# Kernel tuning notes

Measured on AMD Instinct MI355X. Metric: run time of the kernel, lower is better.

Reference implementation:

```python
import jax, jax.numpy as jnp
import numpy as np
from jax import lax

C = 512          # in_channels
L = 4            # fcos_conv_layers
NUM_CLS = 1      # fcos_num_class - 1
PRIOR_BIAS = float(-np.log((1 - 0.01) / 0.01))
BN_EPS = 1e-5


def conv1d(x, w, b, pad):
    # x: [B, Cin, T], w: [Cout, Cin, K]
    y = lax.conv_general_dilated(x, w, window_strides=(1,), padding=[(pad, pad)],
                                 dimension_numbers=('NCH', 'OIH', 'NCH'))
    return y + b[None, :, None]


def bn(x, g, b, m, v):
    inv = lax.rsqrt(v + BN_EPS)
    return (x - m[None, :, None]) * (g * inv)[None, :, None] + b[None, :, None]


def tower(x, ws, bs, gs, bes, ms, vs):
    # ws: [L, C, C, 3]; fixed small loop over layers
    for i in range(L):
        x = jax.nn.relu(bn(conv1d(x, ws[i], bs[i], 1), gs[i], bes[i], ms[i], vs[i]))
    return x


def setup_inputs() -> dict:
    key = jax.random.key(0)
    ks = jax.random.split(key, 32)
    d = {}
    d['f0'] = jax.random.normal(ks[0], (8, C, 1024), jnp.float32)
    d['f1'] = jax.random.normal(ks[1], (8, C, 512), jnp.float32)
    d['f2'] = jax.random.normal(ks[2], (8, C, 256), jnp.float32)

    def nrm(k, shape):
        return 0.01 * jax.random.normal(k, shape, jnp.float32)

    # cls / bbox towers: stacked conv + BN params
    d['cls_tw_w'] = nrm(ks[3], (L, C, C, 3)); d['cls_tw_b'] = jnp.zeros((L, C))
    d['cls_bn_g'] = jnp.ones((L, C)); d['cls_bn_b'] = jnp.zeros((L, C))
    d['cls_bn_m'] = jnp.zeros((L, C)); d['cls_bn_v'] = jnp.ones((L, C))
    d['box_tw_w'] = nrm(ks[4], (L, C, C, 3)); d['box_tw_b'] = jnp.zeros((L, C))
    d['box_bn_g'] = jnp.ones((L, C)); d['box_bn_b'] = jnp.zeros((L, C))
    d['box_bn_m'] = jnp.zeros((L, C)); d['box_bn_v'] = jnp.ones((L, C))

    d['logits_w'] = nrm(ks[5], (NUM_CLS, C, 3))
    d['logits_b'] = jnp.full((NUM_CLS,), PRIOR_BIAS, jnp.float32)
    d['bbox_w'] = nrm(ks[6], (2, C, 3)); d['bbox_b'] = jnp.zeros((2,))

    d['mix_w'] = nrm(ks[7], (C, 2 * C, 1)); d['mix_b'] = jnp.zeros((C,))
    d['mix_bn_g'] = jnp.ones((C,)); d['mix_bn_b'] = jnp.zeros((C,))
    d['mix_bn_m'] = jnp.zeros((C,)); d['mix_bn_v'] = jnp.ones((C,))

    d['iou_w1'] = nrm(ks[8], (C // 2, C, 3)); d['iou_b1'] = jnp.zeros((C // 2,))
    d['iou_bn_g'] = jnp.ones((C // 2,)); d['iou_bn_b'] = jnp.zeros((C // 2,))
    d['iou_bn_m'] = jnp.zeros((C // 2,)); d['iou_bn_v'] = jnp.ones((C // 2,))
    d['iou_w2'] = nrm(ks[9], (1, C // 2, 1)); d['iou_b2'] = jnp.zeros((1,))

    d['scales'] = jnp.ones((3,), jnp.float32)
    return d


def reference(f0, f1, f2,
              cls_tw_w, cls_tw_b, cls_bn_g, cls_bn_b, cls_bn_m, cls_bn_v,
              box_tw_w, box_tw_b, box_bn_g, box_bn_b, box_bn_m, box_bn_v,
              logits_w, logits_b, bbox_w, bbox_b,
              mix_w, mix_b, mix_bn_g, mix_bn_b, mix_bn_m, mix_bn_v,
              iou_w1, iou_b1, iou_bn_g, iou_bn_b, iou_bn_m, iou_bn_v,
              iou_w2, iou_b2, scales):
    outs = []
    for l, x in enumerate([f0, f1, f2]):
        ct = tower(x, cls_tw_w, cls_tw_b, cls_bn_g, cls_bn_b, cls_bn_m, cls_bn_v)
        bt = tower(x, box_tw_w, box_tw_b, box_bn_g, box_bn_b, box_bn_m, box_bn_v)
        logits = conv1d(ct, logits_w, logits_b, 1)                      # [B, 1, T]
        bbox = jnp.exp(conv1d(bt, bbox_w, bbox_b, 1) * scales[l])       # [B, 2, T]
        mix = jax.nn.relu(bn(conv1d(jnp.concatenate([ct, bt], axis=1), mix_w, mix_b, 0),
                             mix_bn_g, mix_bn_b, mix_bn_m, mix_bn_v))   # [B, C, T]
        h = jax.nn.relu(bn(conv1d(mix, iou_w1, iou_b1, 1),
                           iou_bn_g, iou_bn_b, iou_bn_m, iou_bn_v))
        iou = conv1d(h, iou_w2, iou_b2, 0)                              # [B, 1, T]
        outs.append(jnp.concatenate([logits, bbox, iou], axis=1))       # [B, 4, T]
    return jnp.concatenate(outs, axis=-1)  # [B, 4, T0+T1+T2]
```

## Files before the change

kernel.cpp:

```cpp
#include <hip/hip_runtime.h>
#include <hip/hip_bf16.h>


typedef __bf16 bf16x8 __attribute__((ext_vector_type(8)));
typedef float f32x4 __attribute__((ext_vector_type(4)));

__device__ __forceinline__ float bf2f(unsigned short u) {
    union { unsigned int i; float f; } c; c.i = ((unsigned int)u) << 16; return c.f;
}
__device__ __forceinline__ unsigned short f2bf(float f) {
    union { __hip_bfloat16 h; unsigned short u; } c; c.h = __float2bfloat16(f); return c.u;
}

__device__ __forceinline__ void gload16(const void* g, void* l) {
    __builtin_amdgcn_global_load_lds(
        (const __attribute__((address_space(1))) unsigned int*)g,
        (__attribute__((address_space(3))) unsigned int*)l,
        16, 0, 0);
}

__device__ __forceinline__ void tile_decode(int ct, int& rowstart, int& t0, int& Tl) {
    if (ct < 64)      { Tl = 1024; int b = ct >> 3;                 t0 = (ct & 7) << 7; rowstart = b * 1026 + 1; }
    else if (ct < 96) { Tl = 512;  int i = ct - 64; int b = i >> 2; t0 = (i & 3) << 7; rowstart = 8208 + b * 514 + 1; }
    else              { Tl = 256;  int i = ct - 96; int b = i >> 1; t0 = (i & 1) << 7; rowstart = 12320 + b * 258 + 1; }
}

template<int KSIZE>
__global__ __launch_bounds__(256)
void conv_gemm(const unsigned short* __restrict__ X, int xstride, int ci0_base, int ci_twstride, int Cin,
               const unsigned short* __restrict__ W, int w_twstride,
               const float* __restrict__ Bs, int b_twstride,
               unsigned short* __restrict__ Y, int ystride, int co_twstride,
               int relu)
{
    constexpr int BM = 128, BN = 128, BK = 32;
    constexpr int NR = BN + KSIZE - 1;
    constexpr int XSEG = (NR * 64 + 1023) / 1024;
    constexpr int XPW  = (XSEG + 3) / 4;
    constexpr int WSEG = KSIZE * BM * 64 / 1024;
    constexpr int WPW  = WSEG / 4;
    __shared__ alignas(16) unsigned short Xs[2 * XSEG * 512];
    __shared__ alignas(16) unsigned short Ws[2 * WSEG * 512];

    const int tid = threadIdx.x;
    const int lane = tid & 63, wid = tid >> 6;
    int rowstart, t0, Tl;
    tile_decode(blockIdx.x, rowstart, t0, Tl);
    const int co0 = blockIdx.y * BM;
    const int tw = blockIdx.z;
    const int ci_off = ci0_base + tw * ci_twstride;
    const unsigned short* Wp = W + (size_t)tw * w_twstride;
    const float* Bp = Bs + tw * b_twstride;
    const int co_out0 = tw * co_twstride + co0;

    const int wm = (wid >> 1) * 64, wn = (wid & 1) * 64;
    const int lr = lane & 15;
    const int sr = lane >> 4;

    const unsigned short* xga[XPW]; unsigned short* xl[XPW];
#pragma unroll
    for (int p = 0; p < XPW; ++p) {
        int seg = (KSIZE == 3) ? ((p < 2) ? p * 4 + wid : 8) : (p * 4 + wid);
        xl[p] = Xs + seg * 512;
        int g = seg * 64 + lane;
        int row = g >> 2, s = (g & 3) ^ ((row >> 1) & 3);
        xga[p] = X + (size_t)(rowstart - (KSIZE >> 1) + row) * xstride + ci_off + s * 8;
    }
    const unsigned short* wga[WPW]; unsigned short* wl[WPW];
#pragma unroll
    for (int p = 0; p < WPW; ++p) {
        int seg = p * 4 + wid;
        wl[p] = Ws + seg * 512;
        int g = seg * 64 + lane;
        int row = g >> 2, s = (g & 3) ^ ((row >> 1) & 3);
        int co = row & (BM - 1), kk = row >> 7;
        wga[p] = Wp + (size_t)(co0 + co) * (KSIZE * Cin) + kk * Cin + s * 8;
    }

    f32x4 acc[4][4];
#pragma unroll
    for (int i = 0; i < 4; ++i)
#pragma unroll
        for (int j = 0; j < 4; ++j) acc[i][j] = (f32x4){0.f, 0.f, 0.f, 0.f};

    auto STAGE = [&](int buf) {
#pragma unroll
        for (int p = 0; p < XPW; ++p) { gload16(xga[p], xl[p] + buf * (XSEG * 512)); xga[p] += BK; }
#pragma unroll
        for (int p = 0; p < WPW; ++p) { gload16(wga[p], wl[p] + buf * (WSEG * 512)); wga[p] += BK; }
    };

    const int nk = Cin / BK;
    STAGE(0);
    int cur = 0;
    for (int ks = 0; ks < nk; ++ks) {
        if (ks + 1 < nk) {
            STAGE(cur ^ 1);
            if constexpr (KSIZE == 3) asm volatile("s_waitcnt vmcnt(9)" ::: "memory");
            else                      asm volatile("s_waitcnt vmcnt(4)" ::: "memory");
        } else {
            asm volatile("s_waitcnt vmcnt(0)" ::: "memory");
        }
        __builtin_amdgcn_sched_barrier(0);
        __builtin_amdgcn_s_barrier();

        const char* bXs = (const char*)Xs + cur * (XSEG * 1024);
        const char* bWs = (const char*)Ws + cur * (WSEG * 1024);
#pragma unroll
        for (int kk = 0; kk < KSIZE; ++kk) {
            bf16x8 af[4], bv[4];
#pragma unroll
            for (int mi = 0; mi < 4; ++mi) {
                int ra = kk * BM + wm + mi * 16 + lr;
                af[mi] = *(const bf16x8*)(bWs + ra * 64 + (((sr ^ (ra >> 1)) & 3) << 4));
                int rb = wn + mi * 16 + lr + kk;
                bv[mi] = *(const bf16x8*)(bXs + rb * 64 + (((sr ^ (rb >> 1)) & 3) << 4));
            }
#pragma unroll
            for (int mi = 0; mi < 4; ++mi)
#pragma unroll
                for (int ni = 0; ni < 4; ++ni)
                    acc[mi][ni] = __builtin_amdgcn_mfma_f32_16x16x32_bf16(af[mi], bv[ni], acc[mi][ni], 0, 0, 0);
        }
        __builtin_amdgcn_sched_barrier(0);
        __builtin_amdgcn_s_barrier();
        cur ^= 1;
    }

    const int r4 = (lane >> 4) * 4;
#pragma unroll
    for (int mi = 0; mi < 4; ++mi) {
        int co_l = wm + mi * 16 + r4;
        float b0 = Bp[co0 + co_l + 0], b1 = Bp[co0 + co_l + 1];
        float b2 = Bp[co0 + co_l + 2], b3 = Bp[co0 + co_l + 3];
#pragma unroll
        for (int ni = 0; ni < 4; ++ni) {
            int t = t0 + wn + ni * 16 + lr;
            f32x4 a = acc[mi][ni];
            float v0 = a[0] + b0, v1 = a[1] + b1, v2 = a[2] + b2, v3 = a[3] + b3;
            if (relu) {
                v0 = fmaxf(v0, 0.f); v1 = fmaxf(v1, 0.f);
                v2 = fmaxf(v2, 0.f); v3 = fmaxf(v3, 0.f);
            }
            union { unsigned long long u; unsigned short s[4]; } pk;
            pk.s[0] = f2bf(v0); pk.s[1] = f2bf(v1); pk.s[2] = f2bf(v2); pk.s[3] = f2bf(v3);
            *(unsigned long long*)(Y + (size_t)(rowstart + t) * ystride + co_out0 + co_l) = pk.u;
        }
    }
}

__global__ __launch_bounds__(256)
void zero_pads(unsigned short* __restrict__ act0, unsigned short* __restrict__ catA,
               unsigned short* __restrict__ catB, unsigned short* __restrict__ mixo,
               unsigned short* __restrict__ iouh)
{
    int c = blockIdx.x >> 1, side = blockIdx.x & 1;
    int start, Tl;
    if (c < 8)       { start = c * 1026;               Tl = 1024; }
    else if (c < 16) { start = 8208 + (c - 8) * 514;   Tl = 512;  }
    else             { start = 12320 + (c - 16) * 258; Tl = 256;  }
    size_t prow = start + (side ? Tl + 1 : 0);
    int tid = threadIdx.x;
    uint4 z = make_uint4(0u, 0u, 0u, 0u);
    if (tid < 64)  *(uint4*)(act0 + prow * 512 + tid * 8) = z;
    if (tid < 128) { *(uint4*)(catA + prow * 1024 + tid * 8) = z;
                     *(uint4*)(catB + prow * 1024 + tid * 8) = z; }
    if (tid >= 128 && tid < 192) *(uint4*)(mixo + prow * 512 + (tid - 128) * 8) = z;
    if (tid >= 192 && tid < 224) *(uint4*)(iouh + prow * 256 + (tid - 192) * 8) = z;
}

__global__ __launch_bounds__(256)
void transpose_in(const float* __restrict__ f0, const float* __restrict__ f1, const float* __restrict__ f2,
                  unsigned short* __restrict__ act0)
{
    __shared__ float tile[32][33];
    int bx = blockIdx.x;
    const float* src; int Tl, padbase, b, t0;
    if (bx < 256)      { src = f0; Tl = 1024; int i = bx;       b = i >> 5; t0 = (i & 31) << 5; padbase = b * 1026; }
    else if (bx < 384) { src = f1; Tl = 512;  int i = bx - 256; b = i >> 4; t0 = (i & 15) << 5; padbase = 8208 + b * 514; }
    else               { src = f2; Tl = 256;  int i = bx - 384; b = i >> 3; t0 = (i & 7)  << 5; padbase = 12320 + b * 258; }
    int c0 = blockIdx.y << 5;
    const float* sb = src + (size_t)b * 512 * Tl;
    int tl = threadIdx.x & 31, cl = threadIdx.x >> 5;
#pragma unroll
    for (int j = 0; j < 4; ++j) {
        int c = cl + j * 8;
        tile[c][tl] = sb[(size_t)(c0 + c) * Tl + t0 + tl];
    }
    __syncthreads();
    int cc = threadIdx.x & 31, tr0 = threadIdx.x >> 5;
    size_t base = (size_t)(padbase + 1 + t0) * 512 + c0;
#pragma unroll
    for (int j = 0; j < 4; ++j) {
        int tr = tr0 + j * 8;
        act0[base + (size_t)tr * 512 + cc] = f2bf(tile[cc][tr]);
    }
}

__global__ __launch_bounds__(256)
void prep_tower(const float* __restrict__ cls_w, const float* __restrict__ box_w,
                const float* __restrict__ cg, const float* __restrict__ cvv,
                const float* __restrict__ bg, const float* __restrict__ bvv,
                unsigned short* __restrict__ Wt)
{
    int idx = blockIdx.x * 256 + threadIdx.x;
    if (idx >= 2 * 4 * 512 * 3 * 512) return;
    int ci = idx & 511;
    int kk = (idx >> 9) % 3;
    int co = (idx / 1536) & 511;
    int l  = (idx / 786432) & 3;
    int tw = idx / 3145728;
    const float* w = tw ? box_w : cls_w;
    const float* g = tw ? bg : cg;
    const float* v = tw ? bvv : cvv;
    float s = g[l * 512 + co] * rsqrtf(v[l * 512 + co] + 1e-5f);
    float val = w[(((size_t)(l * 512 + co)) * 512 + ci) * 3 + kk] * s;
    Wt[idx] = f2bf(val);
}

__global__ __launch_bounds__(256)
void prep_misc(const float* mix_w, const float* mix_b, const float* mg, const float* mbeta, const float* mm, const float* mv,
               const float* iou_w1, const float* iou_b1, const float* ig, const float* ibeta, const float* im, const float* iv,
               const float* cls_b, const float* cg, const float* cbeta, const float* cm, const float* cv2,
               const float* box_b, const float* bg, const float* bbeta, const float* bm, const float* bv2,
               unsigned short* Wmix, unsigned short* Wiou, float* Bt, float* Bmix, float* Biou)
{
    int idx = blockIdx.x * 256 + threadIdx.x;
    if (idx < 524288) {
        int co = idx >> 10;
        float s = mg[co] * rsqrtf(mv[co] + 1e-5f);
        Wmix[idx] = f2bf(mix_w[idx] * s);
        return;
    }
    idx -= 524288;
    if (idx < 393216) {
        int ci = idx & 511, kk = (idx >> 9) % 3, co = idx / 1536;
        float s = ig[co] * rsqrtf(iv[co] + 1e-5f);
        Wiou[idx] = f2bf(iou_w1[((size_t)(co * 512 + ci)) * 3 + kk] * s);
        return;
    }
    idx -= 393216;
    if (idx < 4096) {
        int co = idx & 511, l = (idx >> 9) & 3, tw = idx >> 11;
        const float* g = tw ? bg : cg; const float* v = tw ? bv2 : cv2;
        const float* m = tw ? bm : cm; const float* be = tw ? bbeta : cbeta;
        const float* cb = tw ? box_b : cls_b;
        int o = l * 512 + co;
        float s = g[o] * rsqrtf(v[o] + 1e-5f);
        Bt[idx] = (cb[o] - m[o]) * s + be[o];
        return;
    }
    idx -= 4096;
    if (idx < 512) {
        float s = mg[idx] * rsqrtf(mv[idx] + 1e-5f);
        Bmix[idx] = (mix_b[idx] - mm[idx]) * s + mbeta[idx];
        return;
    }
    idx -= 512;
    if (idx < 256) {
        float s = ig[idx] * rsqrtf(iv[idx] + 1e-5f);
        Biou[idx] = (iou_b1[idx] - im[idx]) * s + ibeta[idx];
    }
}

__global__ __launch_bounds__(256)
void heads_kernel(const unsigned short* __restrict__ catb, const unsigned short* __restrict__ iouh,
                  const float* __restrict__ lw, const float* __restrict__ lb,
                  const float* __restrict__ bw, const float* __restrict__ bb,
                  const float* __restrict__ iw, const float* __restrict__ ib,
                  const float* __restrict__ scales, float* __restrict__ out)
{
    const int lane = threadIdx.x & 63;
    const int wid = threadIdx.x >> 6;

    float lwr[24], bwr0[24], bwr1[24], iwr[4];
    {
        const float4* p = (const float4*)(lw + lane * 24);
#pragma unroll
        for (int q = 0; q < 6; ++q) {
            float4 v = p[q];
            lwr[q * 4 + 0] = v.x; lwr[q * 4 + 1] = v.y; lwr[q * 4 + 2] = v.z; lwr[q * 4 + 3] = v.w;
        }
        p = (const float4*)(bw + lane * 24);
#pragma unroll
        for (int q = 0; q < 6; ++q) {
            float4 v = p[q];
            bwr0[q * 4 + 0] = v.x; bwr0[q * 4 + 1] = v.y; bwr0[q * 4 + 2] = v.z; bwr0[q * 4 + 3] = v.w;
        }
        p = (const float4*)(bw + 1536 + lane * 24);
#pragma unroll
        for (int q = 0; q < 6; ++q) {
            float4 v = p[q];
            bwr1[q * 4 + 0] = v.x; bwr1[q * 4 + 1] = v.y; bwr1[q * 4 + 2] = v.z; bwr1[q * 4 + 3] = v.w;
        }
        float4 v = *(const float4*)(iw + lane * 4);
        iwr[0] = v.x; iwr[1] = v.y; iwr[2] = v.z; iwr[3] = v.w;
    }
    const float lb0 = lb[0], bb0 = bb[0], bb1 = bb[1], ib0 = ib[0];
    const float s0 = scales[0], s1 = scales[1], s2 = scales[2];

    for (int r = blockIdx.x * 4 + wid; r < 14336; r += gridDim.x * 4) {
        int tlog, roff, tgoff, padbase; float sc;
        if (r < 8192)       { tlog = 10; roff = 0;     tgoff = 0;    sc = s0; }
        else if (r < 12288) { tlog = 9;  roff = 8192;  tgoff = 1024; sc = s1; }
        else                { tlog = 8;  roff = 12288; tgoff = 1536; sc = s2; }
        int i = r - roff;
        int Tl = 1 << tlog;
        int b = i >> tlog, t = i & (Tl - 1);
        if (r < 8192)       padbase = b * 1026;
        else if (r < 12288) padbase = 8208 + b * 514;
        else                padbase = 12320 + b * 258;
        int prow = padbase + 1 + t;

        float al = 0.f, a0 = 0.f, a1 = 0.f, ai = 0.f;
        const unsigned short* base = catb + (size_t)prow * 1024 + lane * 8;
#pragma unroll
        for (int kk = 0; kk < 3; ++kk) {
            union { uint4 u; unsigned short s[8]; } cv, bv;
            cv.u = *(const uint4*)(base + (kk - 1) * 1024);
            bv.u = *(const uint4*)(base + (kk - 1) * 1024 + 512);
#pragma unroll
            for (int j = 0; j < 8; ++j) {
                float xc = bf2f(cv.s[j]);
                float xb = bf2f(bv.s[j]);
                al = fmaf(xc, lwr[j * 3 + kk], al);
                a0 = fmaf(xb, bwr0[j * 3 + kk], a0);
                a1 = fmaf(xb, bwr1[j * 3 + kk], a1);
            }
        }
        {
            union { uint2 u; unsigned short s[4]; } hv;
            hv.u = *(const uint2*)(iouh + (size_t)prow * 256 + lane * 4);
#pragma unroll
            for (int j = 0; j < 4; ++j) ai = fmaf(bf2f(hv.s[j]), iwr[j], ai);
        }
#pragma unroll
        for (int off = 32; off > 0; off >>= 1) {
            al += __shfl_xor(al, off);
            a0 += __shfl_xor(a0, off);
            a1 += __shfl_xor(a1, off);
            ai += __shfl_xor(ai, off);
        }
        if (lane == 0) {
            int tg = tgoff + t;
            out[((size_t)b * 4 + 0) * 1792 + tg] = al + lb0;
            out[((size_t)b * 4 + 1) * 1792 + tg] = expf((a0 + bb0) * sc);
            out[((size_t)b * 4 + 2) * 1792 + tg] = expf((a1 + bb1) * sc);
            out[((size_t)b * 4 + 3) * 1792 + tg] = ai + ib0;
        }
    }
}

extern "C" void kernel_launch(void* const* d_in, const int* in_sizes, int n_in,
                              void* d_out, int out_size, void* d_ws, size_t ws_size,
                              hipStream_t stream)
{
    const float* f0       = (const float*)d_in[0];
    const float* f1       = (const float*)d_in[1];
    const float* f2       = (const float*)d_in[2];
    const float* cls_tw_w = (const float*)d_in[3];
    const float* cls_tw_b = (const float*)d_in[4];
    const float* cls_bn_g = (const float*)d_in[5];
    const float* cls_bn_b = (const float*)d_in[6];
    const float* cls_bn_m = (const float*)d_in[7];
    const float* cls_bn_v = (const float*)d_in[8];
    const float* box_tw_w = (const float*)d_in[9];
    const float* box_tw_b = (const float*)d_in[10];
    const float* box_bn_g = (const float*)d_in[11];
    const float* box_bn_b = (const float*)d_in[12];
    const float* box_bn_m = (const float*)d_in[13];
    const float* box_bn_v = (const float*)d_in[14];
    const float* logits_w = (const float*)d_in[15];
    const float* logits_b = (const float*)d_in[16];
    const float* bbox_w   = (const float*)d_in[17];
    const float* bbox_b   = (const float*)d_in[18];
    const float* mix_w    = (const float*)d_in[19];
    const float* mix_b    = (const float*)d_in[20];
    const float* mix_bn_g = (const float*)d_in[21];
    const float* mix_bn_b = (const float*)d_in[22];
    const float* mix_bn_m = (const float*)d_in[23];
    const float* mix_bn_v = (const float*)d_in[24];
    const float* iou_w1   = (const float*)d_in[25];
    const float* iou_b1   = (const float*)d_in[26];
    const float* iou_bn_g = (const float*)d_in[27];
    const float* iou_bn_b = (const float*)d_in[28];
    const float* iou_bn_m = (const float*)d_in[29];
    const float* iou_bn_v = (const float*)d_in[30];
    const float* iou_w2   = (const float*)d_in[31];
    const float* iou_b2   = (const float*)d_in[32];
    const float* scales   = (const float*)d_in[33];

    unsigned char* ws = (unsigned char*)d_ws;
    unsigned short* Wt   = (unsigned short*)(ws + 0);
    unsigned short* Wmix = (unsigned short*)(ws + 12582912);
    unsigned short* Wiou = (unsigned short*)(ws + 13631488);
    float*          Bt   = (float*)(ws + 14417920);
    float*          Bmix = (float*)(ws + 14434304);
    float*          Biou = (float*)(ws + 14436352);
    unsigned short* act0 = (unsigned short*)(ws + 14437376);
    unsigned short* catA = (unsigned short*)(ws + 29182976);
    unsigned short* catB = (unsigned short*)(ws + 58674176);
    unsigned short* mixo = (unsigned short*)(ws + 88165376);
    unsigned short* iouh = (unsigned short*)(ws + 102910976);

    zero_pads<<<dim3(48), dim3(256), 0, stream>>>(act0, catA, catB, mixo, iouh);
    prep_tower<<<dim3(24576), dim3(256), 0, stream>>>(cls_tw_w, box_tw_w, cls_bn_g, cls_bn_v,
                                                      box_bn_g, box_bn_v, Wt);
    prep_misc<<<dim3(3603), dim3(256), 0, stream>>>(mix_w, mix_b, mix_bn_g, mix_bn_b, mix_bn_m, mix_bn_v,
                                                    iou_w1, iou_b1, iou_bn_g, iou_bn_b, iou_bn_m, iou_bn_v,
                                                    cls_tw_b, cls_bn_g, cls_bn_b, cls_bn_m, cls_bn_v,
                                                    box_tw_b, box_bn_g, box_bn_b, box_bn_m, box_bn_v,
                                                    Wmix, Wiou, Bt, Bmix, Biou);
    transpose_in<<<dim3(448, 16), dim3(256), 0, stream>>>(f0, f1, f2, act0);

    conv_gemm<3><<<dim3(112, 4, 2), 256, 0, stream>>>(act0, 512, 0, 0, 512,
                                                      Wt, 3145728, Bt, 2048, catA, 1024, 512, 1);
    conv_gemm<3><<<dim3(112, 4, 2), 256, 0, stream>>>(catA, 1024, 0, 512, 512,
                                                      Wt + 786432, 3145728, Bt + 512, 2048, catB, 1024, 512, 1);
    conv_gemm<3><<<dim3(112, 4, 2), 256, 0, stream>>>(catB, 1024, 0, 512, 512,
                                                      Wt + 1572864, 3145728, Bt + 1024, 2048, catA, 1024, 512, 1);
    conv_gemm<3><<<dim3(112, 4, 2), 256, 0, stream>>>(catA, 1024, 0, 512, 512,
                                                      Wt + 2359296, 3145728, Bt + 1536, 2048, catB, 1024, 512, 1);
    conv_gemm<1><<<dim3(112, 4, 1), 256, 0, stream>>>(catB, 1024, 0, 0, 1024,
                                                      Wmix, 0, Bmix, 0, mixo, 512, 0, 1);
    conv_gemm<3><<<dim3(112, 2, 1), 256, 0, stream>>>(mixo, 512, 0, 0, 512,
                                                      Wiou, 0, Biou, 0, iouh, 256, 0, 1);
    heads_kernel<<<dim3(896), dim3(256), 0, stream>>>(catB, iouh, logits_w, logits_b,
                                                      bbox_w, bbox_b, iou_w2, iou_b2, scales,
                                                      (float*)d_out);
}
```

Measured before the change: 317.2 us.

## Add dedicated 256x256-tile double-buffered conv kernel for tower layers

Replaces the generic 128x128 conv_gemm launches for the four tower layers with a specialized conv_tower kernel. It uses 512 threads, 256 output channels by 256 time steps per block, and double-buffered LDS with swizzled layouts. Weight loads are interleaved across the three kernel taps, and MFMA runs under raised priority. The larger tiles cut redundant global loads and raise MFMA density, and the remapped block index (L&7)*28+(L>>3) spreads work across XCDs. In exchange, each block uses about 130KB of LDS and many registers, which limits occupancy, and the grid shrinks to 224 blocks, which may leave some CUs underused.

```diff
diff --git a/kernel.cpp b/kernel.cpp
--- a/kernel.cpp
+++ b/kernel.cpp
@@ -17,6 +17,137 @@
         (const __attribute__((address_space(1))) unsigned int*)g,
         (__attribute__((address_space(3))) unsigned int*)l,
         16, 0, 0);
+}
+
+__global__ __launch_bounds__(512, 2)
+void conv_tower(const unsigned short* __restrict__ X, int xstride, int ci_twstride,
+                const unsigned short* __restrict__ W,
+                const float* __restrict__ Bs,
+                unsigned short* __restrict__ Y)
+{
+    constexpr int XHALF = 17 * 512;
+    constexpr int WHALF = 48 * 512;
+    __shared__ alignas(16) unsigned short Xs[2 * XHALF];
+    __shared__ alignas(16) unsigned short Wsh[2 * WHALF];
+
+    const int L = blockIdx.x;
+    const int P = (L & 7) * 28 + (L >> 3);
+    const int tt = P >> 2, sub = P & 3;
+    const int tw = sub >> 1, co0 = (sub & 1) << 8;
+
+    int rowstart;
+    if (tt < 32)      { rowstart = (tt >> 2) * 1026 + 1 + ((tt & 3) << 8); }
+    else if (tt < 48) { int i = tt - 32; rowstart = 8208 + (i >> 1) * 514 + 1 + ((i & 1) << 8); }
+    else              { rowstart = 12320 + (tt - 48) * 258 + 1; }
+
+    const int tid = threadIdx.x;
+    const int lane = tid & 63, wid = tid >> 6;
+    const int wco = (wid >> 2) << 7;
+    const int wt  = (wid & 3) << 6;
+    const int lr = lane & 15;
+    const int sr = lane >> 4;
+
+    const unsigned short* Wp = W + (size_t)tw * 3145728;
+    const float* Bp = Bs + tw * 2048;
+    const int co_out0 = tw * 512 + co0;
+    const int ci_off = tw * ci_twstride;
+
+    const unsigned short* xga[3]; unsigned short* xl0[3];
+#pragma unroll
+    for (int p = 0; p < 3; ++p) {
+        int seg = (p < 2) ? (p * 8 + wid) : 16;
+        xl0[p] = Xs + seg * 512;
+        int g = seg * 64 + lane;
+        int row = g >> 2, sc = (g & 3) ^ ((row >> 1) & 3);
+        xga[p] = X + (size_t)(rowstart - 1 + row) * xstride + ci_off + sc * 8;
+    }
+    const unsigned short* wga[6]; unsigned short* wl0[6];
+#pragma unroll
+    for (int p = 0; p < 6; ++p) {
+        int seg = p * 8 + wid;
+        wl0[p] = Wsh + seg * 512;
+        int g = seg * 64 + lane;
+        int row = g >> 2, sc = (g & 3) ^ ((row >> 1) & 3);
+        int co = row & 255, kk = row >> 8;
+        wga[p] = Wp + (size_t)(co0 + co) * 1536 + kk * 512 + sc * 8;
+    }
+
+    f32x4 acc[8][4];
+#pragma unroll
+    for (int i = 0; i < 8; ++i)
+#pragma unroll
+        for (int j = 0; j < 4; ++j) acc[i][j] = (f32x4){0.f, 0.f, 0.f, 0.f};
+
+#pragma unroll
+    for (int p = 0; p < 3; ++p) { gload16(xga[p], xl0[p]); xga[p] += 32; }
+#pragma unroll
+    for (int p = 0; p < 6; ++p) { gload16(wga[p], wl0[p]); wga[p] += 32; }
+    asm volatile("s_waitcnt vmcnt(0)" ::: "memory");
+    __builtin_amdgcn_s_barrier();
+
+    int cur = 0;
+    for (int ks = 0; ks < 16; ++ks) {
+        const bool notlast = (ks < 15);
+        const char* bX = (const char*)Xs + cur * (XHALF * 2);
+        const char* bW = (const char*)Wsh + cur * (WHALF * 2);
+#pragma unroll
+        for (int kk = 0; kk < 3; ++kk) {
+            bf16x8 af[8], bv[4];
+#pragma unroll
+            for (int mi = 0; mi < 8; ++mi) {
+                int ra = kk * 256 + wco + mi * 16 + lr;
+                af[mi] = *(const bf16x8*)(bW + ra * 64 + (((sr ^ (ra >> 1)) & 3) << 4));
+            }
+#pragma unroll
+            for (int ni = 0; ni < 4; ++ni) {
+                int rb = wt + ni * 16 + lr + kk;
+                bv[ni] = *(const bf16x8*)(bX + rb * 64 + (((sr ^ (rb >> 1)) & 3) << 4));
+            }
+            if (notlast) {
+                if (kk == 0) {
+#pragma unroll
+                    for (int p = 0; p < 3; ++p) { gload16(xga[p], xl0[p] + (cur ^ 1) * XHALF); xga[p] += 32; }
+                } else {
+#pragma unroll
+                    for (int p = 0; p < 3; ++p) {
+                        int q = (kk - 1) * 3 + p;
+                        gload16(wga[q], wl0[q] + (cur ^ 1) * WHALF); wga[q] += 32;
+                    }
+                }
+            }
+            __builtin_amdgcn_s_barrier();
+            asm volatile("s_waitcnt lgkmcnt(0)" ::: "memory");
+            __builtin_amdgcn_sched_barrier(0);
+            __builtin_amdgcn_s_setprio(1);
+#pragma unroll
+            for (int mi = 0; mi < 8; ++mi)
+#pragma unroll
+                for (int ni = 0; ni < 4; ++ni)
+                    acc[mi][ni] = __builtin_amdgcn_mfma_f32_16x16x32_bf16(af[mi], bv[ni], acc[mi][ni], 0, 0, 0);
+            __builtin_amdgcn_s_setprio(0);
+        }
+        if (notlast) asm volatile("s_waitcnt vmcnt(0)" ::: "memory");
+        __builtin_amdgcn_s_barrier();
+        cur ^= 1;
+    }
+
+    const int r4 = sr * 4;
+#pragma unroll
+    for (int mi = 0; mi < 8; ++mi) {
+        int co_l = wco + mi * 16 + r4;
+        float b0 = Bp[co0 + co_l + 0], b1 = Bp[co0 + co_l + 1];
+        float b2 = Bp[co0 + co_l + 2], b3 = Bp[co0 + co_l + 3];
+#pragma unroll
+        for (int ni = 0; ni < 4; ++ni) {
+            int t = wt + ni * 16 + lr;
+            f32x4 a = acc[mi][ni];
+            float v0 = fmaxf(a[0] + b0, 0.f), v1 = fmaxf(a[1] + b1, 0.f);
+            float v2 = fmaxf(a[2] + b2, 0.f), v3 = fmaxf(a[3] + b3, 0.f);
+            union { unsigned long long u; unsigned short s[4]; } pk;
+            pk.s[0] = f2bf(v0); pk.s[1] = f2bf(v1); pk.s[2] = f2bf(v2); pk.s[3] = f2bf(v3);
+            *(unsigned long long*)(Y + (size_t)(rowstart + t) * 1024 + co_out0 + co_l) = pk.u;
+        }
+    }
 }
 
 __device__ __forceinline__ void tile_decode(int ct, int& rowstart, int& t0, int& Tl) {
@@ -413,14 +544,10 @@
                                                     Wmix, Wiou, Bt, Bmix, Biou);
     transpose_in<<<dim3(448, 16), dim3(256), 0, stream>>>(f0, f1, f2, act0);
 
-    conv_gemm<3><<<dim3(112, 4, 2), 256, 0, stream>>>(act0, 512, 0, 0, 512,
-                                                      Wt, 3145728, Bt, 2048, catA, 1024, 512, 1);
-    conv_gemm<3><<<dim3(112, 4, 2), 256, 0, stream>>>(catA, 1024, 0, 512, 512,
-                                                      Wt + 786432, 3145728, Bt + 512, 2048, catB, 1024, 512, 1);
-    conv_gemm<3><<<dim3(112, 4, 2), 256, 0, stream>>>(catB, 1024, 0, 512, 512,
-                                                      Wt + 1572864, 3145728, Bt + 1024, 2048, catA, 1024, 512, 1);
-    conv_gemm<3><<<dim3(112, 4, 2), 256, 0, stream>>>(catA, 1024, 0, 512, 512,
-                                                      Wt + 2359296, 3145728, Bt + 1536, 2048, catB, 1024, 512, 1);
+    conv_tower<<<dim3(224), dim3(512), 0, stream>>>(act0, 512, 0,   Wt,            Bt,        catA);
+    conv_tower<<<dim3(224), dim3(512), 0, stream>>>(catA, 1024, 512, Wt + 786432,  Bt + 512,  catB);
+    conv_tower<<<dim3(224), dim3(512), 0, stream>>>(catB, 1024, 512, Wt + 1572864, Bt + 1024, catA);
+    conv_tower<<<dim3(224), dim3(512), 0, stream>>>(catA, 1024, 512, Wt + 2359296, Bt + 1536, catB);
     conv_gemm<1><<<dim3(112, 4, 1), 256, 0, stream>>>(catB, 1024, 0, 0, 1024,
                                                       Wmix, 0, Bmix, 0, mixo, 512, 0, 1);
     conv_gemm<3><<<dim3(112, 2, 1), 256, 0, stream>>>(mixo, 512, 0, 0, 512,
```

Result: faster. 293.1 us (-7.6%).
